# Optimization experiments

Measured on AMD Instinct MI355X. Metric: run time of the kernel, lower is better.

Reference implementation:

```python
import jax, jax.numpy as jnp
import numpy as np

SOS = 1
H = 1024   # hidden_size
V = 32000  # vocab_size
B = 64     # batch
S = 50     # encoder (source) length
T = 25     # decode steps (target length)


def setup_inputs() -> dict:
    key = jax.random.key(0)
    ks = jax.random.split(key, 16)
    s = 1.0 / np.sqrt(H)

    def u(k, shape):
        return jax.random.uniform(k, shape, jnp.float32, -s, s)

    return {
        "encoder_outputs": jax.random.normal(ks[0], (B, S, H), jnp.float32),
        "encoder_hidden": jax.random.normal(ks[1], (1, B, H), jnp.float32),
        "target_tensor": jax.random.randint(ks[2], (B, T), 0, V),
        "emb": jax.random.normal(ks[3], (V, H), jnp.float32),       # nn.Embedding
        "Wa": u(ks[4], (H, H)), "ba": u(ks[5], (H,)),               # attention query proj
        "Ua": u(ks[6], (H, H)), "bu": u(ks[7], (H,)),               # attention key proj
        "Va": u(ks[8], (H, 1)), "bv": u(ks[9], (1,)),               # attention score vector
        "W_ih": u(ks[10], (3 * H, 2 * H)), "b_ih": u(ks[11], (3 * H,)),  # GRU input weights
        "W_hh": u(ks[12], (3 * H, H)), "b_hh": u(ks[13], (3 * H,)),     # GRU hidden weights
        "Wout": u(ks[14], (V, H)), "bout": u(ks[15], (V,)),         # output linear
    }


def reference(encoder_outputs, encoder_hidden, target_tensor, emb,
              Wa, ba, Ua, bu, Va, bv, W_ih, b_ih, W_hh, b_hh, Wout, bout):
    # Bahdanau key projection is independent of the decode step: precompute once.
    keys_proj = encoder_outputs @ Ua.T + bu        # [B, S, H]
    h0 = encoder_hidden[0]                         # [B, H]

    # Teacher forcing: input at step i is SOS then target[:, :-1]. (Dropout in eval mode = identity.)
    sos = jnp.full((B, 1), SOS, dtype=target_tensor.dtype)
    tokens = jnp.concatenate([sos, target_tensor[:, :-1]], axis=1).T  # [T, B]

    def step(h, tok):
        x_emb = emb[tok]                                         # [B, H]
        q = h @ Wa.T + ba                                        # [B, H] (query = hidden)
        scores = jnp.tanh(q[:, None, :] + keys_proj) @ Va        # [B, S, 1]
        w = jax.nn.softmax(scores[..., 0] + bv[0], axis=-1)      # [B, S]
        context = jnp.einsum('bs,bsh->bh', w, encoder_outputs)   # [B, H]
        x = jnp.concatenate([x_emb, context], axis=-1)           # [B, 2H]
        gx = x @ W_ih.T + b_ih                                   # [B, 3H]
        gh = h @ W_hh.T + b_hh                                   # [B, 3H]
        rx, zx, nx = jnp.split(gx, 3, axis=-1)                   # PyTorch gate order r,z,n
        rh, zh, nh = jnp.split(gh, 3, axis=-1)
        r = jax.nn.sigmoid(rx + rh)
        z = jax.nn.sigmoid(zx + zh)
        n = jnp.tanh(nx + r * nh)
        h_new = (1.0 - z) * n + z * h
        logits = h_new @ Wout.T + bout                           # [B, V]
        return h_new, logits

    _, logits = jax.lax.scan(step, h0, tokens)                   # [T, B, V]
    return jnp.transpose(logits, (1, 0, 2))                      # [B, T, V]
```

## Files before the change

### kernel.cpp

```cpp
#include <hip/hip_runtime.h>
#include <hip/hip_bf16.h>

#define BB_ 64
#define SS_ 50
#define TT_ 25
#define HH_ 1024
#define VV_ 32000

typedef __bf16 bf16x8 __attribute__((ext_vector_type(8)));
typedef float f32x4 __attribute__((ext_vector_type(4)));

__device__ __forceinline__ unsigned short f2b(float f) {
  unsigned u = __float_as_uint(f);
  u = (u + 0x7FFFu + ((u >> 16) & 1u)) >> 16;
  return (unsigned short)u;
}
__device__ __forceinline__ float fast_tanh(float x) {
  float e = __expf(2.f * x);
  return 1.f - 2.f / (e + 1.f);
}
__device__ __forceinline__ float fast_sigmoid(float x) {
  return 1.f / (1.f + __expf(-x));
}
__device__ __forceinline__ void gload16(const void* g, void* l) {
  __builtin_amdgcn_global_load_lds((const __attribute__((address_space(1))) void*)g,
                                   (__attribute__((address_space(3))) void*)l, 16, 0, 0);
}
__device__ __forceinline__ bf16x8 ldb8(const unsigned short* p) {
  return *(const bf16x8*)p;
}

__global__ __launch_bounds__(256) void cvt_bf16(const float* __restrict__ src,
                                                unsigned short* __restrict__ dst, long n) {
  long i = ((long)blockIdx.x * 256 + threadIdx.x) * 4;
  if (i >= n) return;
  float4 v = *(const float4*)(src + i);
  *(ushort4*)(dst + i) = make_ushort4(f2b(v.x), f2b(v.y), f2b(v.z), f2b(v.w));
}

__global__ __launch_bounds__(256) void embed_gather(const int* __restrict__ tgt,
                                                    const float* __restrict__ emb,
                                                    unsigned short* __restrict__ X) {
  long idx = ((long)blockIdx.x * 256 + threadIdx.x) * 4;
  if (idx >= (long)1600 * HH_) return;
  int col = (int)(idx & (HH_ - 1));
  int r = (int)(idx >> 10);
  int t = r % 25;
  int tok = (t == 0) ? 1 : tgt[r - 1];
  float4 v = *(const float4*)(emb + (long)tok * HH_ + col);
  *(ushort4*)(X + idx) = make_ushort4(f2b(v.x), f2b(v.y), f2b(v.z), f2b(v.w));
}

__global__ __launch_bounds__(256) void init_h(const float* __restrict__ eh,
                                              float* __restrict__ Hf,
                                              unsigned short* __restrict__ Hb) {
  int i = (blockIdx.x * 256 + threadIdx.x) * 4;
  if (i >= BB_ * HH_) return;
  float4 v = *(const float4*)(eh + i);
  *(float4*)(Hf + i) = v;
  *(ushort4*)(Hb + i) = make_ushort4(f2b(v.x), f2b(v.y), f2b(v.z), f2b(v.w));
}

__global__ __launch_bounds__(256) void gemm128_bt(
    const unsigned short* __restrict__ A, const unsigned short* __restrict__ W,
    const float* __restrict__ bias, float* __restrict__ out, long ldo,
    int Mtiles, int ldw, int Mvalid) {
  __shared__ __align__(16) unsigned short As[128 * 32];
  __shared__ __align__(16) unsigned short Bs[128 * 32];
  int bid = blockIdx.x;
  int m0 = (bid % Mtiles) * 128;
  int n0 = (bid / Mtiles) * 128;
  int tid = threadIdx.x;
  int w = tid >> 6, l = tid & 63;
  int srow = tid >> 2, scg = tid & 3;
  int mw = (w & 1) * 64, nw = (w >> 1) * 64;

  const unsigned short* Ag0 = A + (long)(m0 + srow) * 1024 + scg * 8;
  const unsigned short* Ag1 = Ag0 + 64 * 1024;
  const unsigned short* Wg0 = W + (long)(n0 + srow) * ldw + scg * 8;
  const unsigned short* Wg1 = Wg0 + (long)64 * ldw;
  unsigned short* lA0 = As + tid * 8;
  unsigned short* lA1 = As + 2048 + tid * 8;
  unsigned short* lB0 = Bs + tid * 8;
  unsigned short* lB1 = Bs + 2048 + tid * 8;

  f32x4 zero = {0.f, 0.f, 0.f, 0.f};
  f32x4 acc[4][4];
#pragma unroll
  for (int i = 0; i < 4; ++i)
#pragma unroll
    for (int j = 0; j < 4; ++j) acc[i][j] = zero;

  for (int k0 = 0; k0 < 1024; k0 += 32) {
    __syncthreads();
    gload16(Ag0 + k0, lA0);
    gload16(Ag1 + k0, lA1);
    gload16(Wg0 + k0, lB0);
    gload16(Wg1 + k0, lB1);
    __syncthreads();
    bf16x8 af[4], bg[4];
#pragma unroll
    for (int mt = 0; mt < 4; ++mt)
      af[mt] = ldb8(As + (mw + mt * 16 + (l & 15)) * 32 + (l >> 4) * 8);
#pragma unroll
    for (int nt = 0; nt < 4; ++nt)
      bg[nt] = ldb8(Bs + (nw + nt * 16 + (l & 15)) * 32 + (l >> 4) * 8);
#pragma unroll
    for (int mt = 0; mt < 4; ++mt)
#pragma unroll
      for (int nt = 0; nt < 4; ++nt)
        acc[mt][nt] = __builtin_amdgcn_mfma_f32_16x16x32_bf16(af[mt], bg[nt], acc[mt][nt], 0, 0, 0);
  }

  int lr = (l >> 4) * 4, lc = l & 15;
#pragma unroll
  for (int nt = 0; nt < 4; ++nt) {
    int col = n0 + nw + nt * 16 + lc;
    float bv = bias[col];
#pragma unroll
    for (int mt = 0; mt < 4; ++mt) {
#pragma unroll
      for (int r = 0; r < 4; ++r) {
        int m = m0 + mw + mt * 16 + lr + r;
        if (m < Mvalid) out[(long)m * ldo + col] = acc[mt][nt][r] + bv;
      }
    }
  }
}

__global__ __launch_bounds__(256) void step_qgh(
    const unsigned short* __restrict__ Hb, const unsigned short* __restrict__ WaB,
    const unsigned short* __restrict__ WhhB, const float* __restrict__ ba,
    const float* __restrict__ bhh, float* __restrict__ Q, float* __restrict__ GH) {
  int gw = (int)((blockIdx.x * blockDim.x + threadIdx.x) >> 6);
  int l = threadIdx.x & 63;
  int m0 = (gw & 3) * 16;
  int n = (gw >> 2) * 16;
  const unsigned short* Wp;
  const float* bp;
  float* op;
  long ldo;
  if (n < 1024) { Wp = WaB + (long)n * 1024; bp = ba + n; op = Q + n; ldo = 1024; }
  else { int n2 = n - 1024; Wp = WhhB + (long)n2 * 1024; bp = bhh + n2; op = GH + n2; ldo = 3072; }
  const unsigned short* Ap = Hb + (long)(m0 + (l & 15)) * 1024 + (l >> 4) * 8;
  const unsigned short* Bp = Wp + (long)(l & 15) * 1024 + (l >> 4) * 8;
  f32x4 acc = {0.f, 0.f, 0.f, 0.f};
#pragma unroll 4
  for (int k = 0; k < 1024; k += 32)
    acc = __builtin_amdgcn_mfma_f32_16x16x32_bf16(ldb8(Ap + k), ldb8(Bp + k), acc, 0, 0, 0);
  int lc = l & 15, lr = (l >> 4) * 4;
  float bv = bp[lc];
#pragma unroll
  for (int r = 0; r < 4; ++r) op[(long)(m0 + lr + r) * ldo + lc] = acc[r] + bv;
}

__global__ __launch_bounds__(512) void step_attn(
    const float* __restrict__ Q, const float* __restrict__ KEYS,
    const float* __restrict__ Va, const float* __restrict__ enc,
    float* __restrict__ CTX, unsigned short* __restrict__ Cb) {
  int b = blockIdx.x;
  int tid = threadIdx.x, w = tid >> 6, l = tid & 63;
  __shared__ float sc[64];
  __shared__ float wgt[64];
  const float* q = Q + (long)b * HH_;
  const float* kbase = KEYS + (long)b * SS_ * HH_;
  for (int s = w; s < SS_; s += 8) {
    const float* kr = kbase + (long)s * HH_;
    float p = 0.f;
#pragma unroll
    for (int j = 0; j < 16; ++j) {
      int hh = l + j * 64;
      p += fast_tanh(q[hh] + kr[hh]) * Va[hh];
    }
#pragma unroll
    for (int off = 32; off; off >>= 1) p += __shfl_down(p, off);
    if (l == 0) sc[s] = p;
  }
  __syncthreads();
  if (tid < 64) {
    float v = (tid < SS_) ? sc[tid] : -1e30f;
    float m = v;
#pragma unroll
    for (int off = 32; off; off >>= 1) m = fmaxf(m, __shfl_down(m, off));
    m = __shfl(m, 0);
    float e = (tid < SS_) ? __expf(v - m) : 0.f;
    float ssum = e;
#pragma unroll
    for (int off = 32; off; off >>= 1) ssum += __shfl_down(ssum, off);
    ssum = __shfl(ssum, 0);
    if (tid < SS_) wgt[tid] = e / ssum;
  }
  __syncthreads();
  for (int c = tid; c < HH_; c += 512) {
    float a0 = 0.f;
    const float* ep = enc + (long)b * SS_ * HH_ + c;
#pragma unroll 10
    for (int s = 0; s < SS_; ++s) a0 += wgt[s] * ep[(long)s * HH_];
    CTX[(long)b * HH_ + c] = a0;
    Cb[(long)b * HH_ + c] = f2b(a0);
  }
}

__global__ __launch_bounds__(256) void step_gru(
    const unsigned short* __restrict__ Cb, const unsigned short* __restrict__ WihB,
    const float* __restrict__ GA, const float* __restrict__ GH,
    float* __restrict__ Hf, unsigned short* __restrict__ Hb,
    unsigned short* __restrict__ HALL, int t) {
  int gw = (int)((blockIdx.x * blockDim.x + threadIdx.x) >> 6);
  int l = threadIdx.x & 63;
  int m0 = (gw & 3) * 16;
  int n0 = (gw >> 2) * 16;
  const unsigned short* Ap = Cb + (long)(m0 + (l & 15)) * 1024 + (l >> 4) * 8;
  const unsigned short* B0 = WihB + (long)(n0 + (l & 15)) * 2048 + 1024 + (l >> 4) * 8;
  const unsigned short* B1 = B0 + (long)1024 * 2048;
  const unsigned short* B2 = B0 + (long)2048 * 2048;
  f32x4 ar = {0.f, 0.f, 0.f, 0.f}, az = ar, an = ar;
#pragma unroll 4
  for (int k = 0; k < 1024; k += 32) {
    bf16x8 a = ldb8(Ap + k);
    ar = __builtin_amdgcn_mfma_f32_16x16x32_bf16(a, ldb8(B0 + k), ar, 0, 0, 0);
    az = __builtin_amdgcn_mfma_f32_16x16x32_bf16(a, ldb8(B1 + k), az, 0, 0, 0);
    an = __builtin_amdgcn_mfma_f32_16x16x32_bf16(a, ldb8(B2 + k), an, 0, 0, 0);
  }
  int lc = l & 15, lr = (l >> 4) * 4;
  int i = n0 + lc;
#pragma unroll
  for (int r = 0; r < 4; ++r) {
    int bb = m0 + lr + r;
    long rowBT = (long)bb * 25 + t;
    const float* ga = GA + rowBT * 3072;
    const float* gh = GH + (long)bb * 3072;
    float rr = fast_sigmoid(ga[i] + ar[r] + gh[i]);
    float zz = fast_sigmoid(ga[1024 + i] + az[r] + gh[1024 + i]);
    float nn = fast_tanh(ga[2048 + i] + an[r] + rr * gh[2048 + i]);
    float hold = Hf[(long)bb * 1024 + i];
    float hnew = (1.f - zz) * nn + zz * hold;
    Hf[(long)bb * 1024 + i] = hnew;
    unsigned short hb = f2b(hnew);
    Hb[(long)bb * 1024 + i] = hb;
    HALL[rowBT * 1024 + i] = hb;
  }
}

extern "C" void kernel_launch(void* const* d_in, const int* in_sizes, int n_in,
                              void* d_out, int out_size, void* d_ws, size_t ws_size,
                              hipStream_t stream) {
  (void)in_sizes; (void)n_in; (void)out_size; (void)ws_size;
  const float* enc  = (const float*)d_in[0];
  const float* ehid = (const float*)d_in[1];
  const int*   tgt  = (const int*)d_in[2];
  const float* emb  = (const float*)d_in[3];
  const float* Wa   = (const float*)d_in[4];
  const float* ba   = (const float*)d_in[5];
  const float* Ua   = (const float*)d_in[6];
  const float* bu   = (const float*)d_in[7];
  const float* Va   = (const float*)d_in[8];
  const float* Wih  = (const float*)d_in[10];
  const float* bih  = (const float*)d_in[11];
  const float* Whh  = (const float*)d_in[12];
  const float* bhh  = (const float*)d_in[13];
  const float* Wout = (const float*)d_in[14];
  const float* bout = (const float*)d_in[15];
  float* out = (float*)d_out;

  char* p = (char*)d_ws;
  auto alloc = [&](size_t bytes) { char* r = p; p += (bytes + 255) & ~(size_t)255; return r; };
  unsigned short* WOUTB = (unsigned short*)alloc((size_t)VV_ * HH_ * 2);
  unsigned short* WIHB  = (unsigned short*)alloc((size_t)3072 * 2048 * 2);
  unsigned short* WHHB  = (unsigned short*)alloc((size_t)3072 * 1024 * 2);
  unsigned short* WAB   = (unsigned short*)alloc((size_t)1024 * 1024 * 2);
  unsigned short* UAB   = (unsigned short*)alloc((size_t)1024 * 1024 * 2);
  unsigned short* ENCB  = (unsigned short*)alloc((size_t)BB_ * SS_ * HH_ * 2);
  unsigned short* XEMB  = (unsigned short*)alloc((size_t)1664 * HH_ * 2);
  unsigned short* HALLB = (unsigned short*)alloc((size_t)1664 * HH_ * 2);
  float* KEYS = (float*)alloc((size_t)BB_ * SS_ * HH_ * 4);
  float* GA   = (float*)alloc((size_t)1600 * 3072 * 4);
  float* GHf  = (float*)alloc((size_t)BB_ * 3072 * 4);
  float* Qf   = (float*)alloc((size_t)BB_ * HH_ * 4);
  float* Hf   = (float*)alloc((size_t)BB_ * HH_ * 4);
  unsigned short* Hb = (unsigned short*)alloc((size_t)BB_ * HH_ * 2);
  float* CTX  = (float*)alloc((size_t)BB_ * HH_ * 4);
  unsigned short* CTXB = (unsigned short*)alloc((size_t)BB_ * HH_ * 2);

  auto cvt = [&](const float* s, unsigned short* d, long n) {
    cvt_bf16<<<dim3((unsigned)((n / 4 + 255) / 256)), dim3(256), 0, stream>>>(s, d, n);
  };
  cvt(Wout, WOUTB, (long)VV_ * HH_);
  cvt(Wih, WIHB, (long)3072 * 2048);
  cvt(Whh, WHHB, (long)3072 * 1024);
  cvt(Wa, WAB, (long)1024 * 1024);
  cvt(Ua, UAB, (long)1024 * 1024);
  cvt(enc, ENCB, (long)BB_ * SS_ * HH_);
  embed_gather<<<dim3(1600 * HH_ / 4 / 256), dim3(256), 0, stream>>>(tgt, emb, XEMB);
  init_h<<<dim3(BB_ * HH_ / 4 / 256), dim3(256), 0, stream>>>(ehid, Hf, Hb);

  gemm128_bt<<<dim3(25 * 8), dim3(256), 0, stream>>>(ENCB, UAB, bu, KEYS, (long)1024, 25, 1024, 3200);
  gemm128_bt<<<dim3(13 * 24), dim3(256), 0, stream>>>(XEMB, WIHB, bih, GA, (long)3072, 13, 2048, 1600);

  for (int t = 0; t < TT_; ++t) {
    step_qgh<<<dim3(256), dim3(256), 0, stream>>>(Hb, WAB, WHHB, ba, bhh, Qf, GHf);
    step_attn<<<dim3(64), dim3(512), 0, stream>>>(Qf, KEYS, Va, enc, CTX, CTXB);
    step_gru<<<dim3(64), dim3(256), 0, stream>>>(CTXB, WIHB, GA, GHf, Hf, Hb, HALLB, t);
  }

  gemm128_bt<<<dim3(13 * 250), dim3(256), 0, stream>>>(HALLB, WOUTB, bout, out, (long)VV_, 13, 1024, 1600);
}
```

Measured before the change: 1.818 ms.

## Fuse per-step RNN kernels into one cooperative persistent kernel with grid syncs

Replaces the 75 per-step launches (q/gh projection, attention, GRU) with a single cooperative kernel of 256 blocks that loops over the decode steps and separates phases with grid.sync(). Attention now reads bf16 copies of the keys and encoder outputs, which halves the bytes read per step but adds an extra conversion pass and some precision loss. The GEMM's shared-memory reads use an XOR swizzle to reduce bank conflicts. The intent is to remove launch overhead and serialization gaps, at the cost of grid-wide barriers and only 64 blocks being active in the attention and GRU phases.

```diff
diff --git a/kernel.cpp b/kernel.cpp
--- a/kernel.cpp
+++ b/kernel.cpp
@@ -1,5 +1,8 @@
 #include <hip/hip_runtime.h>
 #include <hip/hip_bf16.h>
+#include <hip/hip_cooperative_groups.h>
+
+namespace cg = cooperative_groups;
 
 #define BB_ 64
 #define SS_ 50
@@ -14,6 +17,9 @@
   unsigned u = __float_as_uint(f);
   u = (u + 0x7FFFu + ((u >> 16) & 1u)) >> 16;
   return (unsigned short)u;
+}
+__device__ __forceinline__ float b2f(unsigned short u) {
+  return __uint_as_float((unsigned)u << 16);
 }
 __device__ __forceinline__ float fast_tanh(float x) {
   float e = __expf(2.f * x);
@@ -73,11 +79,13 @@
   int tid = threadIdx.x;
   int w = tid >> 6, l = tid & 63;
   int srow = tid >> 2, scg = tid & 3;
+  int xr = (srow >> 1) & 3;
   int mw = (w & 1) * 64, nw = (w >> 1) * 64;
-
-  const unsigned short* Ag0 = A + (long)(m0 + srow) * 1024 + scg * 8;
+  int lc = l & 15, lq = l >> 4;
+
+  const unsigned short* Ag0 = A + (long)(m0 + srow) * 1024 + (scg ^ xr) * 8;
   const unsigned short* Ag1 = Ag0 + 64 * 1024;
-  const unsigned short* Wg0 = W + (long)(n0 + srow) * ldw + scg * 8;
+  const unsigned short* Wg0 = W + (long)(n0 + srow) * ldw + (scg ^ xr) * 8;
   const unsigned short* Wg1 = Wg0 + (long)64 * ldw;
   unsigned short* lA0 = As + tid * 8;
   unsigned short* lA1 = As + 2048 + tid * 8;
@@ -100,11 +108,15 @@
     __syncthreads();
     bf16x8 af[4], bg[4];
 #pragma unroll
-    for (int mt = 0; mt < 4; ++mt)
-      af[mt] = ldb8(As + (mw + mt * 16 + (l & 15)) * 32 + (l >> 4) * 8);
-#pragma unroll
-    for (int nt = 0; nt < 4; ++nt)
-      bg[nt] = ldb8(Bs + (nw + nt * 16 + (l & 15)) * 32 + (l >> 4) * 8);
+    for (int mt = 0; mt < 4; ++mt) {
+      int r = mw + mt * 16 + lc;
+      af[mt] = ldb8(As + r * 32 + ((lq ^ ((r >> 1) & 3)) * 8));
+    }
+#pragma unroll
+    for (int nt = 0; nt < 4; ++nt) {
+      int r = nw + nt * 16 + lc;
+      bg[nt] = ldb8(Bs + r * 32 + ((lq ^ ((r >> 1) & 3)) * 8));
+    }
 #pragma unroll
     for (int mt = 0; mt < 4; ++mt)
 #pragma unroll
@@ -112,7 +124,7 @@
         acc[mt][nt] = __builtin_amdgcn_mfma_f32_16x16x32_bf16(af[mt], bg[nt], acc[mt][nt], 0, 0, 0);
   }
 
-  int lr = (l >> 4) * 4, lc = l & 15;
+  int lr = lq * 4;
 #pragma unroll
   for (int nt = 0; nt < 4; ++nt) {
     int col = n0 + nw + nt * 16 + lc;
@@ -128,117 +140,128 @@
   }
 }
 
-__global__ __launch_bounds__(256) void step_qgh(
-    const unsigned short* __restrict__ Hb, const unsigned short* __restrict__ WaB,
-    const unsigned short* __restrict__ WhhB, const float* __restrict__ ba,
-    const float* __restrict__ bhh, float* __restrict__ Q, float* __restrict__ GH) {
-  int gw = (int)((blockIdx.x * blockDim.x + threadIdx.x) >> 6);
-  int l = threadIdx.x & 63;
-  int m0 = (gw & 3) * 16;
-  int n = (gw >> 2) * 16;
-  const unsigned short* Wp;
-  const float* bp;
-  float* op;
-  long ldo;
-  if (n < 1024) { Wp = WaB + (long)n * 1024; bp = ba + n; op = Q + n; ldo = 1024; }
-  else { int n2 = n - 1024; Wp = WhhB + (long)n2 * 1024; bp = bhh + n2; op = GH + n2; ldo = 3072; }
-  const unsigned short* Ap = Hb + (long)(m0 + (l & 15)) * 1024 + (l >> 4) * 8;
-  const unsigned short* Bp = Wp + (long)(l & 15) * 1024 + (l >> 4) * 8;
-  f32x4 acc = {0.f, 0.f, 0.f, 0.f};
-#pragma unroll 4
-  for (int k = 0; k < 1024; k += 32)
-    acc = __builtin_amdgcn_mfma_f32_16x16x32_bf16(ldb8(Ap + k), ldb8(Bp + k), acc, 0, 0, 0);
-  int lc = l & 15, lr = (l >> 4) * 4;
-  float bv = bp[lc];
-#pragma unroll
-  for (int r = 0; r < 4; ++r) op[(long)(m0 + lr + r) * ldo + lc] = acc[r] + bv;
-}
-
-__global__ __launch_bounds__(512) void step_attn(
-    const float* __restrict__ Q, const float* __restrict__ KEYS,
-    const float* __restrict__ Va, const float* __restrict__ enc,
-    float* __restrict__ CTX, unsigned short* __restrict__ Cb) {
-  int b = blockIdx.x;
-  int tid = threadIdx.x, w = tid >> 6, l = tid & 63;
+__global__ __launch_bounds__(256, 1) void rnn_steps(
+    float* __restrict__ Hf, unsigned short* __restrict__ Hb,
+    const unsigned short* __restrict__ WAB, const unsigned short* __restrict__ WHHB,
+    const unsigned short* __restrict__ WIHB,
+    const float* __restrict__ ba, const float* __restrict__ bhh,
+    const unsigned short* __restrict__ KEYSB, const float* __restrict__ Va,
+    const unsigned short* __restrict__ ENCB, const float* __restrict__ GA,
+    float* __restrict__ Qf, float* __restrict__ GHf,
+    unsigned short* __restrict__ CTXB, unsigned short* __restrict__ HALLB) {
+  cg::grid_group grid = cg::this_grid();
+  int gid = blockIdx.x;
+  int tid = threadIdx.x;
+  int w = tid >> 6, l = tid & 63;
+  int lc = l & 15, lq = l >> 4, lr = (l >> 4) * 4;
   __shared__ float sc[64];
   __shared__ float wgt[64];
-  const float* q = Q + (long)b * HH_;
-  const float* kbase = KEYS + (long)b * SS_ * HH_;
-  for (int s = w; s < SS_; s += 8) {
-    const float* kr = kbase + (long)s * HH_;
-    float p = 0.f;
-#pragma unroll
-    for (int j = 0; j < 16; ++j) {
-      int hh = l + j * 64;
-      p += fast_tanh(q[hh] + kr[hh]) * Va[hh];
-    }
-#pragma unroll
-    for (int off = 32; off; off >>= 1) p += __shfl_down(p, off);
-    if (l == 0) sc[s] = p;
-  }
-  __syncthreads();
-  if (tid < 64) {
-    float v = (tid < SS_) ? sc[tid] : -1e30f;
-    float m = v;
-#pragma unroll
-    for (int off = 32; off; off >>= 1) m = fmaxf(m, __shfl_down(m, off));
-    m = __shfl(m, 0);
-    float e = (tid < SS_) ? __expf(v - m) : 0.f;
-    float ssum = e;
-#pragma unroll
-    for (int off = 32; off; off >>= 1) ssum += __shfl_down(ssum, off);
-    ssum = __shfl(ssum, 0);
-    if (tid < SS_) wgt[tid] = e / ssum;
-  }
-  __syncthreads();
-  for (int c = tid; c < HH_; c += 512) {
-    float a0 = 0.f;
-    const float* ep = enc + (long)b * SS_ * HH_ + c;
+
+  const unsigned short* Wp1;
+  const float* bp1;
+  float* op1;
+  long ldo1;
+  {
+    int n = gid * 16;
+    if (n < 1024) { Wp1 = WAB + (long)n * 1024; bp1 = ba + n; op1 = Qf + n; ldo1 = 1024; }
+    else { int n2 = n - 1024; Wp1 = WHHB + (long)n2 * 1024; bp1 = bhh + n2; op1 = GHf + n2; ldo1 = 3072; }
+  }
+  const unsigned short* Ap1 = Hb + (long)(w * 16 + lc) * 1024 + lq * 8;
+  const unsigned short* Bp1 = Wp1 + (long)lc * 1024 + lq * 8;
+  float bv1 = bp1[lc];
+
+  const unsigned short* Ap3 = CTXB + (long)(w * 16 + lc) * 1024 + lq * 8;
+  const unsigned short* B30 = WIHB + (long)(gid * 16 + lc) * 2048 + 1024 + lq * 8;
+  const unsigned short* B31 = B30 + (long)1024 * 2048;
+  const unsigned short* B32 = B30 + (long)2048 * 2048;
+
+  for (int t = 0; t < TT_; ++t) {
+    {
+      f32x4 acc = {0.f, 0.f, 0.f, 0.f};
+#pragma unroll 4
+      for (int k = 0; k < 1024; k += 32)
+        acc = __builtin_amdgcn_mfma_f32_16x16x32_bf16(ldb8(Ap1 + k), ldb8(Bp1 + k), acc, 0, 0, 0);
+#pragma unroll
+      for (int r = 0; r < 4; ++r) op1[(long)(w * 16 + lr + r) * ldo1 + lc] = acc[r] + bv1;
+    }
+    grid.sync();
+
+    if (gid < 64) {
+      int b = gid;
+      const float* q = Qf + (long)b * HH_;
+      const unsigned short* kb = KEYSB + (long)b * SS_ * HH_;
+      for (int s = w; s < SS_; s += 4) {
+        const unsigned short* kr = kb + (long)s * HH_;
+        float p = 0.f;
+#pragma unroll
+        for (int j = 0; j < 16; ++j) {
+          int hh = l + j * 64;
+          p += fast_tanh(q[hh] + b2f(kr[hh])) * Va[hh];
+        }
+#pragma unroll
+        for (int off = 32; off; off >>= 1) p += __shfl_down(p, off);
+        if (l == 0) sc[s] = p;
+      }
+      __syncthreads();
+      if (tid < 64) {
+        float v = (tid < SS_) ? sc[tid] : -1e30f;
+        float m = v;
+#pragma unroll
+        for (int off = 32; off; off >>= 1) m = fmaxf(m, __shfl_down(m, off));
+        m = __shfl(m, 0);
+        float e = (tid < SS_) ? __expf(v - m) : 0.f;
+        float ssum = e;
+#pragma unroll
+        for (int off = 32; off; off >>= 1) ssum += __shfl_down(ssum, off);
+        ssum = __shfl(ssum, 0);
+        if (tid < SS_) wgt[tid] = e / ssum;
+      }
+      __syncthreads();
+      {
+        int c0 = tid * 4;
+        const unsigned short* eb = ENCB + (long)b * SS_ * HH_ + c0;
+        float a0 = 0.f, a1 = 0.f, a2 = 0.f, a3 = 0.f;
 #pragma unroll 10
-    for (int s = 0; s < SS_; ++s) a0 += wgt[s] * ep[(long)s * HH_];
-    CTX[(long)b * HH_ + c] = a0;
-    Cb[(long)b * HH_ + c] = f2b(a0);
-  }
-}
-
-__global__ __launch_bounds__(256) void step_gru(
-    const unsigned short* __restrict__ Cb, const unsigned short* __restrict__ WihB,
-    const float* __restrict__ GA, const float* __restrict__ GH,
-    float* __restrict__ Hf, unsigned short* __restrict__ Hb,
-    unsigned short* __restrict__ HALL, int t) {
-  int gw = (int)((blockIdx.x * blockDim.x + threadIdx.x) >> 6);
-  int l = threadIdx.x & 63;
-  int m0 = (gw & 3) * 16;
-  int n0 = (gw >> 2) * 16;
-  const unsigned short* Ap = Cb + (long)(m0 + (l & 15)) * 1024 + (l >> 4) * 8;
-  const unsigned short* B0 = WihB + (long)(n0 + (l & 15)) * 2048 + 1024 + (l >> 4) * 8;
-  const unsigned short* B1 = B0 + (long)1024 * 2048;
-  const unsigned short* B2 = B0 + (long)2048 * 2048;
-  f32x4 ar = {0.f, 0.f, 0.f, 0.f}, az = ar, an = ar;
+        for (int s = 0; s < SS_; ++s) {
+          ushort4 e = *(const ushort4*)(eb + (long)s * HH_);
+          float ww = wgt[s];
+          a0 += ww * b2f(e.x); a1 += ww * b2f(e.y);
+          a2 += ww * b2f(e.z); a3 += ww * b2f(e.w);
+        }
+        *(ushort4*)(CTXB + (long)b * HH_ + c0) =
+            make_ushort4(f2b(a0), f2b(a1), f2b(a2), f2b(a3));
+      }
+    }
+    grid.sync();
+
+    if (gid < 64) {
+      f32x4 ar = {0.f, 0.f, 0.f, 0.f}, az = ar, an = ar;
 #pragma unroll 4
-  for (int k = 0; k < 1024; k += 32) {
-    bf16x8 a = ldb8(Ap + k);
-    ar = __builtin_amdgcn_mfma_f32_16x16x32_bf16(a, ldb8(B0 + k), ar, 0, 0, 0);
-    az = __builtin_amdgcn_mfma_f32_16x16x32_bf16(a, ldb8(B1 + k), az, 0, 0, 0);
-    an = __builtin_amdgcn_mfma_f32_16x16x32_bf16(a, ldb8(B2 + k), an, 0, 0, 0);
-  }
-  int lc = l & 15, lr = (l >> 4) * 4;
-  int i = n0 + lc;
-#pragma unroll
-  for (int r = 0; r < 4; ++r) {
-    int bb = m0 + lr + r;
-    long rowBT = (long)bb * 25 + t;
-    const float* ga = GA + rowBT * 3072;
-    const float* gh = GH + (long)bb * 3072;
-    float rr = fast_sigmoid(ga[i] + ar[r] + gh[i]);
-    float zz = fast_sigmoid(ga[1024 + i] + az[r] + gh[1024 + i]);
-    float nn = fast_tanh(ga[2048 + i] + an[r] + rr * gh[2048 + i]);
-    float hold = Hf[(long)bb * 1024 + i];
-    float hnew = (1.f - zz) * nn + zz * hold;
-    Hf[(long)bb * 1024 + i] = hnew;
-    unsigned short hb = f2b(hnew);
-    Hb[(long)bb * 1024 + i] = hb;
-    HALL[rowBT * 1024 + i] = hb;
+      for (int k = 0; k < 1024; k += 32) {
+        bf16x8 a = ldb8(Ap3 + k);
+        ar = __builtin_amdgcn_mfma_f32_16x16x32_bf16(a, ldb8(B30 + k), ar, 0, 0, 0);
+        az = __builtin_amdgcn_mfma_f32_16x16x32_bf16(a, ldb8(B31 + k), az, 0, 0, 0);
+        an = __builtin_amdgcn_mfma_f32_16x16x32_bf16(a, ldb8(B32 + k), an, 0, 0, 0);
+      }
+      int i = gid * 16 + lc;
+#pragma unroll
+      for (int r = 0; r < 4; ++r) {
+        int bb = w * 16 + lr + r;
+        long rowBT = (long)bb * 25 + t;
+        const float* ga = GA + rowBT * 3072;
+        const float* gh = GHf + (long)bb * 3072;
+        float rr = fast_sigmoid(ga[i] + ar[r] + gh[i]);
+        float zz = fast_sigmoid(ga[1024 + i] + az[r] + gh[1024 + i]);
+        float nn = fast_tanh(ga[2048 + i] + an[r] + rr * gh[2048 + i]);
+        float hold = Hf[(long)bb * 1024 + i];
+        float hnew = (1.f - zz) * nn + zz * hold;
+        Hf[(long)bb * 1024 + i] = hnew;
+        unsigned short hb = f2b(hnew);
+        Hb[(long)bb * 1024 + i] = hb;
+        HALLB[rowBT * 1024 + i] = hb;
+      }
+    }
+    grid.sync();
   }
 }
 
@@ -274,12 +297,12 @@
   unsigned short* XEMB  = (unsigned short*)alloc((size_t)1664 * HH_ * 2);
   unsigned short* HALLB = (unsigned short*)alloc((size_t)1664 * HH_ * 2);
   float* KEYS = (float*)alloc((size_t)BB_ * SS_ * HH_ * 4);
+  unsigned short* KEYSB = (unsigned short*)alloc((size_t)BB_ * SS_ * HH_ * 2);
   float* GA   = (float*)alloc((size_t)1600 * 3072 * 4);
   float* GHf  = (float*)alloc((size_t)BB_ * 3072 * 4);
   float* Qf   = (float*)alloc((size_t)BB_ * HH_ * 4);
   float* Hf   = (float*)alloc((size_t)BB_ * HH_ * 4);
   unsigned short* Hb = (unsigned short*)alloc((size_t)BB_ * HH_ * 2);
-  float* CTX  = (float*)alloc((size_t)BB_ * HH_ * 4);
   unsigned short* CTXB = (unsigned short*)alloc((size_t)BB_ * HH_ * 2);
 
   auto cvt = [&](const float* s, unsigned short* d, long n) {
@@ -295,12 +318,13 @@
   init_h<<<dim3(BB_ * HH_ / 4 / 256), dim3(256), 0, stream>>>(ehid, Hf, Hb);
 
   gemm128_bt<<<dim3(25 * 8), dim3(256), 0, stream>>>(ENCB, UAB, bu, KEYS, (long)1024, 25, 1024, 3200);
+  cvt(KEYS, KEYSB, (long)BB_ * SS_ * HH_);
   gemm128_bt<<<dim3(13 * 24), dim3(256), 0, stream>>>(XEMB, WIHB, bih, GA, (long)3072, 13, 2048, 1600);
 
-  for (int t = 0; t < TT_; ++t) {
-    step_qgh<<<dim3(256), dim3(256), 0, stream>>>(Hb, WAB, WHHB, ba, bhh, Qf, GHf);
-    step_attn<<<dim3(64), dim3(512), 0, stream>>>(Qf, KEYS, Va, enc, CTX, CTXB);
-    step_gru<<<dim3(64), dim3(256), 0, stream>>>(CTXB, WIHB, GA, GHf, Hf, Hb, HALLB, t);
+  {
+    void* kargs[] = {&Hf, &Hb, &WAB, &WHHB, &WIHB, &ba, &bhh, &KEYSB, &Va,
+                     &ENCB, &GA, &Qf, &GHf, &CTXB, &HALLB};
+    hipLaunchCooperativeKernel((const void*)rnn_steps, dim3(256), dim3(256), kargs, 0, stream);
   }
 
   gemm128_bt<<<dim3(13 * 250), dim3(256), 0, stream>>>(HALLB, WOUTB, bout, out, (long)VV_, 13, 1024, 1600);
```

Measured after the change: 4.911 ms. +170.1%, slower.
